# Kernel optimization log

Measured on AMD Instinct MI355X. Metric: run time of the kernel, lower is better.

Reference implementation:

```python
import jax, jax.numpy as jnp
import numpy as np

B, T = 16, 8192
L, RC, DC, SC, EC, E, NC = 16, 32, 32, 256, 256, 100, 256


def conv1d(x, w, b, dilation=1):
    # x: [B, Cin, T], w: [Cout, Cin, K], b: [Cout]
    y = jax.lax.conv_general_dilated(
        x, w, window_strides=(1,), padding='VALID',
        rhs_dilation=(dilation,), dimension_numbers=('NCH', 'OIH', 'NCH'))
    return y + b[None, :, None]


def setup_inputs() -> dict:
    key = jax.random.key(0)
    ks = jax.random.split(key, 32)
    n = lambda k, shp: (jax.random.normal(k, shp) * 0.1).astype(jnp.float32)
    return dict(
        tokens=jax.random.randint(ks[0], (B, T), 0, NC),
        emb=n(ks[1], (NC, E)),
        init_w=n(ks[2], (RC, E, 1)), init_b=n(ks[3], (RC,)),
        dil_w=n(ks[4], (L, DC, RC, 2)), dil_b=n(ks[5], (L, DC)),
        filt_w=n(ks[6], (L, DC, DC, 2)), filt_b=n(ks[7], (L, DC)),
        gate_w=n(ks[8], (L, DC, DC, 2)), gate_b=n(ks[9], (L, DC)),
        res_w=n(ks[10], (L, RC, DC, 1)), res_b=n(ks[11], (L, RC)),
        skip_w=n(ks[12], (L, SC, DC, 1)), skip_b=n(ks[13], (L, SC)),
        end1_w=n(ks[14], (EC, SC, 1)), end1_b=n(ks[15], (EC,)),
        end2_w=n(ks[16], (EC, EC, 1)), end2_b=n(ks[17], (EC,)),
        fc1_w=n(ks[18], (128, 256)), fc1_b=n(ks[19], (128,)),
        fc2_w=n(ks[20], (128, 128)), fc2_b=n(ks[21], (128,)),
        fc3_w=n(ks[22], (64, 128)), fc3_b=n(ks[23], (64,)),
        fc4_w=n(ks[24], (NC, 64)), fc4_b=n(ks[25], (NC,)),
    )


def reference(tokens, emb, init_w, init_b, dil_w, dil_b, filt_w, filt_b,
              gate_w, gate_b, res_w, res_b, skip_w, skip_b,
              end1_w, end1_b, end2_w, end2_b,
              fc1_w, fc1_b, fc2_w, fc2_b, fc3_w, fc3_b, fc4_w, fc4_b):
    x = emb[tokens]                     # [B, T, E]
    x = jnp.transpose(x, (0, 2, 1))     # [B, E, T]
    x = conv1d(x, init_w, init_b)       # [B, RC, T]
    skip = None
    for i in range(L):
        d = 2 ** (i % 4)                # dilation resets each block of 4 layers
        xp = jnp.pad(x, ((0, 0), (0, 0), (d + 1, 0)))        # left pad d+1
        residual = conv1d(xp, dil_w[i], dil_b[i], dilation=d)  # [B, DC, T+1]
        f = jnp.tanh(conv1d(residual, filt_w[i], filt_b[i]))   # [B, DC, T]
        g = jax.nn.sigmoid(conv1d(residual, gate_w[i], gate_b[i]))
        x = f * g
        skip = conv1d(x, skip_w[i], skip_b[i])   # overwritten each layer (source bug, kept faithful)
        x = conv1d(x, res_w[i], res_b[i]) + residual[:, :, :-1]
    h = jax.nn.relu(conv1d(jax.nn.relu(skip), end1_w, end1_b))
    h = conv1d(h, end2_w, end2_b)       # [B, EC, T]
    h = h[:, :, -1]                     # [B, 256] last timestep only
    h = jax.nn.relu(h @ fc1_w.T + fc1_b)
    h = jax.nn.relu(h @ fc2_w.T + fc2_b)
    h = jax.nn.relu(h @ fc3_w.T + fc3_b)
    out = h @ fc4_w.T + fc4_b           # [B, NC]
    return out
```

## Files before the change

kernel.cpp:

```cpp
#include <hip/hip_runtime.h>


#define BB 16
#define TT 8192
#define LL 16
#define W0 77
#define NT 256

typedef __attribute__((ext_vector_type(8)))  short short8;
typedef __attribute__((ext_vector_type(16))) float float16;

#define MFMA_B16(a, b, c) __builtin_amdgcn_mfma_f32_32x32x16_bf16(a, b, c, 0, 0, 0)

__device__ __forceinline__ short f2bs(float f) {
  union { float ff; unsigned u; } v; v.ff = f;
  unsigned u = v.u;
  return (short)((u + 0x7FFFu + ((u >> 16) & 1u)) >> 16);
}
__device__ __forceinline__ float b2f(short h) {
  union { unsigned u; float f; } v;
  v.u = ((unsigned)(unsigned short)h) << 16; return v.f;
}

__device__ __forceinline__ void afrag2(const short* src, int row, int kh, short8* out) {
  out[0] = *(const short8*)&src[row * 32 + 8 * kh];
  out[1] = *(const short8*)&src[row * 32 + 16 + 8 * kh];
}

__device__ __forceinline__ void load_chunk(
    int li, int cid, float* pf,
    const float* dil_w, const float* filt_w, const float* gate_w, const float* res_w)
{
  int mat = cid >> 7;
  int h = (cid >> 6) & 1, ln = cid & 63;
  int n = ln & 31, k2 = ln >> 5;
  int base = (li * 32 + n) * 32 + 16 * h + 8 * k2;
  if (mat == 6) {
    const float* p = res_w + base;
    #pragma unroll
    for (int j = 0; j < 8; j++) pf[j] = p[j];
  } else {
    const float* w = (mat < 2) ? dil_w : (mat < 4) ? filt_w : gate_w;
    const float* p = w + base * 2 + (mat & 1);
    #pragma unroll
    for (int j = 0; j < 8; j++) pf[j] = p[2 * j];
  }
}

__global__ __launch_bounds__(NT, 1) void wavenet_kernel(
    const int* __restrict__ tokens,
    const float* __restrict__ emb,
    const float* __restrict__ init_w, const float* __restrict__ init_b,
    const float* __restrict__ dil_w,  const float* __restrict__ dil_b,
    const float* __restrict__ filt_w, const float* __restrict__ filt_b,
    const float* __restrict__ gate_w, const float* __restrict__ gate_b,
    const float* __restrict__ res_w,  const float* __restrict__ res_b,
    const float* __restrict__ skip_w, const float* __restrict__ skip_b,
    const float* __restrict__ end1_w, const float* __restrict__ end1_b,
    const float* __restrict__ end2_w, const float* __restrict__ end2_b,
    const float* __restrict__ fc1_w,  const float* __restrict__ fc1_b,
    const float* __restrict__ fc2_w,  const float* __restrict__ fc2_b,
    const float* __restrict__ fc3_w,  const float* __restrict__ fc3_b,
    const float* __restrict__ fc4_w,  const float* __restrict__ fc4_b,
    float* __restrict__ out)
{
  __shared__ __align__(16) short bfw[2][7168];
  __shared__ float bias2[2][128];
  __shared__ __align__(16) short xbuf[W0 * 32];
  __shared__ __align__(16) short pool[8624];
  __shared__ int tok[W0];
  __shared__ __align__(16) float vecA[256], vecB[256];

  short* rb = pool;
  short* xm = pool + 2432;

  const int tid  = threadIdx.x;
  const int lane = tid & 63;
  const int wv   = tid >> 6;
  const int m    = lane & 31;
  const int kh   = lane >> 5;
  const int b    = blockIdx.x;

  if (tid < W0) tok[tid] = tokens[b * TT + (TT - 1 - tid)];
  __syncthreads();

  for (int cid = tid; cid < 77 * 14; cid += NT) {
    int u = cid / 14, s = cid % 14;
    const float* er = emb + tok[u] * 100 + s * 8;
    short8 v;
    if (s < 12) {
      #pragma unroll
      for (int j = 0; j < 8; j++) v[j] = f2bs(er[j]);
    } else if (s == 12) {
      #pragma unroll
      for (int j = 0; j < 4; j++) v[j] = f2bs(er[j]);
      #pragma unroll
      for (int j = 4; j < 8; j++) v[j] = 0;
    } else {
      #pragma unroll
      for (int j = 0; j < 8; j++) v[j] = 0;
    }
    *(short8*)&pool[u * 112 + s * 8] = v;
  }
  for (int cid = tid; cid < 896; cid += NT) {
    float pf[8];
    load_chunk(0, cid, pf, dil_w, filt_w, gate_w, res_w);
    short8 v;
    #pragma unroll
    for (int j = 0; j < 8; j++) v[j] = f2bs(pf[j]);
    *(short8*)&bfw[0][cid * 8] = v;
  }
  if (tid < 128) {
    const float* bsrc = (tid < 32) ? dil_b : (tid < 64) ? filt_b : (tid < 96) ? gate_b : res_b;
    bias2[0][tid] = bsrc[tid & 31];
  }
  __syncthreads();

  if (wv < 3) {
    short8 bi[7];
    #pragma unroll
    for (int s = 0; s < 7; s++) {
      const float* p = init_w + m * 100 + s * 16 + kh * 8;
      short8 v;
      if (s < 6) {
        #pragma unroll
        for (int j = 0; j < 8; j++) v[j] = f2bs(p[j]);
      } else if (kh == 0) {
        #pragma unroll
        for (int j = 0; j < 4; j++) v[j] = f2bs(p[j]);
        #pragma unroll
        for (int j = 4; j < 8; j++) v[j] = 0;
      } else {
        #pragma unroll
        for (int j = 0; j < 8; j++) v[j] = 0;
      }
      bi[s] = v;
    }
    const float binit = init_b[m];
    const int R = wv * 32;
    int u = R + m; if (u > 76) u = 76;
    float16 acc;
    #pragma unroll
    for (int r = 0; r < 16; r++) acc[r] = binit;
    #pragma unroll
    for (int s = 0; s < 7; s++) {
      short8 a = *(const short8*)&pool[u * 112 + s * 16 + kh * 8];
      acc = MFMA_B16(a, bi[s], acc);
    }
    #pragma unroll
    for (int r = 0; r < 16; r++) {
      int row = (r & 3) + 8 * (r >> 2) + 4 * kh;
      int uu = R + row;
      if (uu < W0) xbuf[uu * 32 + m] = f2bs(acc[r]);
    }
  }
  __syncthreads();

  int Win = W0;
  for (int i = 0; i < LL; i++) {
    const int d = 1 << (i & 3);
    const int Wout = Win - d - 1;
    const int T = (Wout + 32) >> 5;
    const short* bw = bfw[i & 1];
    const float* bs = bias2[i & 1];

    float pfo[4][8];
    float pbias = 0.f;
    const int nch = (tid < 128) ? 4 : 3;
    const bool oldpf = (T >= 3) && (i + 1 < LL);
    if (oldpf) {
      #pragma unroll
      for (int q = 0; q < 4; q++) {
        if (q < nch)
          load_chunk(i + 1, tid + q * NT, pfo[q], dil_w, filt_w, gate_w, res_w);
      }
      if (tid < 128) {
        const float* bsrc = (tid < 32) ? dil_b : (tid < 64) ? filt_b : (tid < 96) ? gate_b : res_b;
        pbias = bsrc[(i + 1) * 32 + (tid & 31)];
      }
    }
    const bool newpf = (T <= 2) && (i + 1 < LL) && (wv >= T);
    const int nP = NT - T * 64;
    const int ptid = tid - T * 64;
    float pfn[7][8];
    if (newpf) {
      #pragma unroll
      for (int q = 0; q < 7; q++) {
        int c = ptid + q * nP;
        if (c < 896) load_chunk(i + 1, c, pfn[q], dil_w, filt_w, gate_w, res_w);
      }
    }

    short8 BW[5][2];
    if (wv < T) {
      const int R = wv * 32;
      short8 B0[2], B1[2];
      #pragma unroll
      for (int h = 0; h < 2; h++) {
        B0[h] = *(const short8*)&bw[((0 * 2 + h) * 64 + lane) * 8];
        B1[h] = *(const short8*)&bw[((1 * 2 + h) * 64 + lane) * 8];
      }
      #pragma unroll
      for (int mt = 0; mt < 5; mt++)
        #pragma unroll
        for (int h = 0; h < 2; h++)
          BW[mt][h] = *(const short8*)&bw[(((mt + 2) * 2 + h) * 64 + lane) * 8];
      int vra = R + m + d; if (vra > Win - 1) vra = Win - 1;
      int vrz = R + m;     if (vrz > Win - 1) vrz = Win - 1;
      short8 aA[2], aZ[2];
      afrag2(xbuf, vra, kh, aA);
      afrag2(xbuf, vrz, kh, aZ);
      float16 acc;
      const float bc = bs[m];
      #pragma unroll
      for (int r = 0; r < 16; r++) acc[r] = bc;
      acc = MFMA_B16(aA[0], B0[0], acc);
      acc = MFMA_B16(aA[1], B0[1], acc);
      acc = MFMA_B16(aZ[0], B1[0], acc);
      acc = MFMA_B16(aZ[1], B1[1], acc);
      #pragma unroll
      for (int r = 0; r < 16; r++) {
        int row = (r & 3) + 8 * (r >> 2) + 4 * kh;
        int vr = R + row;
        if (vr <= Wout) rb[vr * 32 + m] = f2bs(acc[r]);
      }
    }
    if (T >= 2) {
      __syncthreads();
    } else {
      asm volatile("s_waitcnt lgkmcnt(0)" ::: "memory");
    }

    if (wv < T) {
      const int R = wv * 32;
      int r1 = R + m + 1; if (r1 > Wout) r1 = Wout;
      int r0 = R + m;     if (r0 > Wout) r0 = Wout;
      short8 a1[2], a0[2];
      afrag2(rb, r1, kh, a1);
      afrag2(rb, r0, kh, a0);
      float16 accF, accG;
      const float bf = bs[32 + m], bg = bs[64 + m];
      #pragma unroll
      for (int r = 0; r < 16; r++) { accF[r] = bf; accG[r] = bg; }
      accF = MFMA_B16(a1[0], BW[0][0], accF);
      accF = MFMA_B16(a1[1], BW[0][1], accF);
      accF = MFMA_B16(a0[0], BW[1][0], accF);
      accF = MFMA_B16(a0[1], BW[1][1], accF);
      accG = MFMA_B16(a1[0], BW[2][0], accG);
      accG = MFMA_B16(a1[1], BW[2][1], accG);
      accG = MFMA_B16(a0[0], BW[3][0], accG);
      accG = MFMA_B16(a0[1], BW[3][1], accG);
      #pragma unroll
      for (int r = 0; r < 16; r++) {
        int row = (r & 3) + 8 * (r >> 2) + 4 * kh;
        int uf = R + row;
        if (uf < Wout) {
          float u = __expf(-2.f * accF[r]);
          float v = __expf(-accG[r]);
          float fg = (1.f - u) * __builtin_amdgcn_rcpf((1.f + u) * (1.f + v));
          xm[uf * 32 + m] = f2bs(fg);
        }
      }
      asm volatile("s_waitcnt lgkmcnt(0)" ::: "memory");

      int rx = R + m; if (rx > Wout - 1) rx = Wout - 1;
      short8 aX[2];
      afrag2(xm, rx, kh, aX);
      float16 accX;
      const float br = bs[96 + m];
      #pragma unroll
      for (int r = 0; r < 16; r++) {
        int row = (r & 3) + 8 * (r >> 2) + 4 * kh;
        int rr = R + row + 1; if (rr > Wout) rr = Wout;
        accX[r] = br + b2f(rb[rr * 32 + m]);
      }
      accX = MFMA_B16(aX[0], BW[4][0], accX);
      accX = MFMA_B16(aX[1], BW[4][1], accX);
      #pragma unroll
      for (int r = 0; r < 16; r++) {
        int row = (r & 3) + 8 * (r >> 2) + 4 * kh;
        int uf = R + row;
        if (uf < Wout) xbuf[uf * 32 + m] = f2bs(accX[r]);
      }
    } else if (newpf) {
      short* dst = bfw[(i + 1) & 1];
      #pragma unroll
      for (int q = 0; q < 7; q++) {
        int c = ptid + q * nP;
        if (c < 896) {
          short8 v;
          #pragma unroll
          for (int j = 0; j < 8; j++) v[j] = f2bs(pfn[q][j]);
          *(short8*)&dst[c * 8] = v;
        }
      }
      for (int t2 = ptid; t2 < 128; t2 += nP) {
        const float* bsrc = (t2 < 32) ? dil_b : (t2 < 64) ? filt_b : (t2 < 96) ? gate_b : res_b;
        bias2[(i + 1) & 1][t2] = bsrc[(i + 1) * 32 + (t2 & 31)];
      }
    }

    if (oldpf) {
      short* dst = bfw[(i + 1) & 1];
      #pragma unroll
      for (int q = 0; q < 4; q++) {
        if (q < nch) {
          short8 v;
          #pragma unroll
          for (int j = 0; j < 8; j++) v[j] = f2bs(pfo[q][j]);
          *(short8*)&dst[(tid + q * NT) * 8] = v;
        }
      }
      if (tid < 128) bias2[(i + 1) & 1][tid] = pbias;
    }
    __syncthreads();
    Win = Wout;
  }

  {
    float acc = skip_b[15 * 256 + tid];
    const float* wr = skip_w + (15 * 256 + tid) * 32;
    #pragma unroll
    for (int k = 0; k < 32; k += 4) {
      float4 w = *(const float4*)&wr[k];
      acc += (w.x * b2f(xm[k]) + w.y * b2f(xm[k+1])) + (w.z * b2f(xm[k+2]) + w.w * b2f(xm[k+3]));
    }
    vecA[tid] = fmaxf(acc, 0.f);
  }
  __syncthreads();
  {
    const float* wr = end1_w + tid * 256;
    float a4[4] = {0.f, 0.f, 0.f, 0.f};
    #pragma unroll 4
    for (int k = 0; k < 256; k += 16) {
      #pragma unroll
      for (int q = 0; q < 4; q++) {
        float4 w = *(const float4*)&wr[k + 4 * q];
        float4 a = *(const float4*)&vecA[k + 4 * q];
        a4[q] += (w.x * a.x + w.y * a.y) + (w.z * a.z + w.w * a.w);
      }
    }
    vecB[tid] = fmaxf(end1_b[tid] + (a4[0] + a4[1]) + (a4[2] + a4[3]), 0.f);
  }
  __syncthreads();
  float h2;
  {
    const float* wr = end2_w + tid * 256;
    float a4[4] = {0.f, 0.f, 0.f, 0.f};
    #pragma unroll 4
    for (int k = 0; k < 256; k += 16) {
      #pragma unroll
      for (int q = 0; q < 4; q++) {
        float4 w = *(const float4*)&wr[k + 4 * q];
        float4 a = *(const float4*)&vecB[k + 4 * q];
        a4[q] += (w.x * a.x + w.y * a.y) + (w.z * a.z + w.w * a.w);
      }
    }
    h2 = end2_b[tid] + (a4[0] + a4[1]) + (a4[2] + a4[3]);
  }
  __syncthreads();
  vecA[tid] = h2;
  __syncthreads();
  if (tid < 128) {
    const float* wr = fc1_w + tid * 256;
    float a4[4] = {0.f, 0.f, 0.f, 0.f};
    #pragma unroll 4
    for (int k = 0; k < 256; k += 16) {
      #pragma unroll
      for (int q = 0; q < 4; q++) {
        float4 w = *(const float4*)&wr[k + 4 * q];
        float4 a = *(const float4*)&vecA[k + 4 * q];
        a4[q] += (w.x * a.x + w.y * a.y) + (w.z * a.z + w.w * a.w);
      }
    }
    vecB[tid] = fmaxf(fc1_b[tid] + (a4[0] + a4[1]) + (a4[2] + a4[3]), 0.f);
  }
  __syncthreads();
  if (tid < 128) {
    const float* wr = fc2_w + tid * 128;
    float a4[4] = {0.f, 0.f, 0.f, 0.f};
    #pragma unroll 2
    for (int k = 0; k < 128; k += 16) {
      #pragma unroll
      for (int q = 0; q < 4; q++) {
        float4 w = *(const float4*)&wr[k + 4 * q];
        float4 a = *(const float4*)&vecB[k + 4 * q];
        a4[q] += (w.x * a.x + w.y * a.y) + (w.z * a.z + w.w * a.w);
      }
    }
    vecA[tid] = fmaxf(fc2_b[tid] + (a4[0] + a4[1]) + (a4[2] + a4[3]), 0.f);
  }
  __syncthreads();
  if (tid < 64) {
    const float* wr = fc3_w + tid * 128;
    float a4[4] = {0.f, 0.f, 0.f, 0.f};
    #pragma unroll 2
    for (int k = 0; k < 128; k += 16) {
      #pragma unroll
      for (int q = 0; q < 4; q++) {
        float4 w = *(const float4*)&wr[k + 4 * q];
        float4 a = *(const float4*)&vecA[k + 4 * q];
        a4[q] += (w.x * a.x + w.y * a.y) + (w.z * a.z + w.w * a.w);
      }
    }
    vecB[tid] = fmaxf(fc3_b[tid] + (a4[0] + a4[1]) + (a4[2] + a4[3]), 0.f);
  }
  __syncthreads();
  {
    const float* wr = fc4_w + tid * 64;
    float a4[4] = {0.f, 0.f, 0.f, 0.f};
    #pragma unroll
    for (int k = 0; k < 64; k += 16) {
      #pragma unroll
      for (int q = 0; q < 4; q++) {
        float4 w = *(const float4*)&wr[k + 4 * q];
        float4 a = *(const float4*)&vecB[k + 4 * q];
        a4[q] += (w.x * a.x + w.y * a.y) + (w.z * a.z + w.w * a.w);
      }
    }
    out[b * 256 + tid] = fc4_b[tid] + (a4[0] + a4[1]) + (a4[2] + a4[3]);
  }
}

extern "C" void kernel_launch(void* const* d_in, const int* in_sizes, int n_in,
                              void* d_out, int out_size, void* d_ws, size_t ws_size,
                              hipStream_t stream) {
  wavenet_kernel<<<BB, NT, 0, stream>>>(
      (const int*)d_in[0],    (const float*)d_in[1],  (const float*)d_in[2],  (const float*)d_in[3],
      (const float*)d_in[4],  (const float*)d_in[5],  (const float*)d_in[6],  (const float*)d_in[7],
      (const float*)d_in[8],  (const float*)d_in[9],  (const float*)d_in[10], (const float*)d_in[11],
      (const float*)d_in[12], (const float*)d_in[13], (const float*)d_in[14], (const float*)d_in[15],
      (const float*)d_in[16], (const float*)d_in[17], (const float*)d_in[18], (const float*)d_in[19],
      (const float*)d_in[20], (const float*)d_in[21], (const float*)d_in[22], (const float*)d_in[23],
      (const float*)d_in[24], (const float*)d_in[25], (float*)d_out);
}
```

Measured before the change: 208.4 us.

## Run last five WaveNet layers in one wavefront with register shuffles

The final five layers now run in a specialized path. When the window is 32 timesteps or fewer, wave 0 holds activations in registers and passes time-shifted operands between lanes with shuffles and packed bf16 conversions, so no LDS round trips are needed. The other three waves prefetch and convert the next layer's weights and biases in parallel. This aims to cut LDS traffic and barrier latency on the small tail layers. The risk is heavy register pressure and leaving the other waves idle during the compute.

```diff
diff --git a/kernel.cpp b/kernel.cpp
--- a/kernel.cpp
+++ b/kernel.cpp
@@ -20,6 +20,28 @@
 __device__ __forceinline__ float b2f(short h) {
   union { unsigned u; float f; } v;
   v.u = ((unsigned)(unsigned short)h) << 16; return v.f;
+}
+__device__ __forceinline__ unsigned cvtpk(float lo, float hi) {
+  unsigned r;
+  asm("v_cvt_pk_bf16_f32 %0, %1, %2" : "=v"(r) : "v"(lo), "v"(hi));
+  return r;
+}
+__device__ __forceinline__ short8 mk8(unsigned a, unsigned b, unsigned c, unsigned d) {
+  union { unsigned u[4]; short8 s; } z;
+  z.u[0] = a; z.u[1] = b; z.u[2] = c; z.u[3] = d; return z.s;
+}
+__device__ __forceinline__ float u2f(unsigned u) {
+  union { unsigned x; float f; } z; z.x = u; return z.f;
+}
+__device__ __forceinline__ void asmb(const unsigned* own, const unsigned* cr,
+                                     int kh, unsigned* o) {
+  #pragma unroll
+  for (int h = 0; h < 2; h++) {
+    o[4*h+0] = kh ? cr[4*h+2] : own[4*h+0];
+    o[4*h+1] = kh ? cr[4*h+3] : own[4*h+1];
+    o[4*h+2] = kh ? own[4*h+2] : cr[4*h+0];
+    o[4*h+3] = kh ? own[4*h+3] : cr[4*h+1];
+  }
 }
 
 __device__ __forceinline__ void afrag2(const short* src, int row, int kh, short8* out) {
@@ -65,7 +87,7 @@
     float* __restrict__ out)
 {
   __shared__ __align__(16) short bfw[2][7168];
-  __shared__ float bias2[2][128];
+  __shared__ __align__(16) float bias2[2][128];
   __shared__ __align__(16) short xbuf[W0 * 32];
   __shared__ __align__(16) short pool[8624];
   __shared__ int tok[W0];
@@ -157,7 +179,7 @@
   __syncthreads();
 
   int Win = W0;
-  for (int i = 0; i < LL; i++) {
+  for (int i = 0; i < 11; i++) {
     const int d = 1 << (i & 3);
     const int Wout = Win - d - 1;
     const int T = (Wout + 32) >> 5;
@@ -315,6 +337,167 @@
     }
     __syncthreads();
     Win = Wout;
+  }
+
+  {
+    const int t31 = lane & 31;
+    const int hb  = lane & 32;
+    unsigned xcur[8];
+    if (wv == 0) {
+      int tcl = t31 < Win - 1 ? t31 : Win - 1;
+      #pragma unroll
+      for (int h = 0; h < 2; h++) {
+        short8 v = *(const short8*)&xbuf[tcl * 32 + 16 * h + 8 * kh];
+        union { short8 s; unsigned u[4]; } z; z.s = v;
+        #pragma unroll
+        for (int s = 0; s < 4; s++) xcur[4 * h + s] = z.u[s];
+      }
+    }
+
+    #pragma unroll
+    for (int i = 11; i < LL; i++) {
+      const int d = 1 << (i & 3);
+      const int Wout = Win - d - 1;
+      const short* bw = bfw[i & 1];
+      const float* bs = bias2[i & 1];
+
+      const bool npf = (i + 1 < LL) && (wv >= 1);
+      const int ptid = tid - 64;
+      float pfn[7][8];
+      if (npf) {
+        #pragma unroll
+        for (int q = 0; q < 7; q++) {
+          int c = ptid + q * 192;
+          if (c < 896) load_chunk(i + 1, c, pfn[q], dil_w, filt_w, gate_w, res_w);
+        }
+      }
+
+      if (wv == 0) {
+        short8 WA[7][2];
+        #pragma unroll
+        for (int mt = 0; mt < 7; mt++)
+          #pragma unroll
+          for (int h = 0; h < 2; h++)
+            WA[mt][h] = *(const short8*)&bw[((mt * 2 + h) * 64 + lane) * 8];
+
+        int td = t31 + d; if (td > Win - 1) td = Win - 1;
+        int srcd = hb | td;
+        unsigned xd[8];
+        #pragma unroll
+        for (int q = 0; q < 8; q++) xd[q] = (unsigned)__shfl((int)xcur[q], srcd);
+        float16 acc;
+        #pragma unroll
+        for (int g = 0; g < 4; g++) {
+          float4 b4 = *(const float4*)&bs[4 * kh + 8 * g];
+          acc[4*g+0] = b4.x; acc[4*g+1] = b4.y; acc[4*g+2] = b4.z; acc[4*g+3] = b4.w;
+        }
+        acc = MFMA_B16(WA[0][0], mk8(xd[0], xd[1], xd[2], xd[3]), acc);
+        acc = MFMA_B16(WA[0][1], mk8(xd[4], xd[5], xd[6], xd[7]), acc);
+        acc = MFMA_B16(WA[1][0], mk8(xcur[0], xcur[1], xcur[2], xcur[3]), acc);
+        acc = MFMA_B16(WA[1][1], mk8(xcur[4], xcur[5], xcur[6], xcur[7]), acc);
+
+        unsigned wrb[8], xc[8], x1[8], x1c[8];
+        #pragma unroll
+        for (int q = 0; q < 8; q++) wrb[q] = cvtpk(acc[2 * q], acc[2 * q + 1]);
+        int t1 = t31 + 1; if (t1 > Wout) t1 = Wout;
+        int s1o = hb | t1;
+        int s1c = (hb ^ 32) | t1;
+        #pragma unroll
+        for (int q = 0; q < 8; q++) {
+          xc[q]  = (unsigned)__shfl((int)wrb[q], lane ^ 32);
+          x1[q]  = (unsigned)__shfl((int)wrb[q], s1o);
+          x1c[q] = (unsigned)__shfl((int)wrb[q], s1c);
+        }
+        unsigned rb0w[8], rb1w[8];
+        asmb(wrb, xc, kh, rb0w);
+        asmb(x1, x1c, kh, rb1w);
+
+        float16 accF, accG;
+        #pragma unroll
+        for (int g = 0; g < 4; g++) {
+          float4 bF = *(const float4*)&bs[32 + 4 * kh + 8 * g];
+          float4 bG = *(const float4*)&bs[64 + 4 * kh + 8 * g];
+          accF[4*g+0] = bF.x; accF[4*g+1] = bF.y; accF[4*g+2] = bF.z; accF[4*g+3] = bF.w;
+          accG[4*g+0] = bG.x; accG[4*g+1] = bG.y; accG[4*g+2] = bG.z; accG[4*g+3] = bG.w;
+        }
+        short8 RB10 = mk8(rb1w[0], rb1w[1], rb1w[2], rb1w[3]);
+        short8 RB11 = mk8(rb1w[4], rb1w[5], rb1w[6], rb1w[7]);
+        short8 RB00 = mk8(rb0w[0], rb0w[1], rb0w[2], rb0w[3]);
+        short8 RB01 = mk8(rb0w[4], rb0w[5], rb0w[6], rb0w[7]);
+        accF = MFMA_B16(WA[2][0], RB10, accF);
+        accF = MFMA_B16(WA[2][1], RB11, accF);
+        accF = MFMA_B16(WA[3][0], RB00, accF);
+        accF = MFMA_B16(WA[3][1], RB01, accF);
+        accG = MFMA_B16(WA[4][0], RB10, accG);
+        accG = MFMA_B16(WA[4][1], RB11, accG);
+        accG = MFMA_B16(WA[5][0], RB00, accG);
+        accG = MFMA_B16(WA[5][1], RB01, accG);
+        float fg[16];
+        #pragma unroll
+        for (int r = 0; r < 16; r++) {
+          float u = __expf(-2.f * accF[r]);
+          float v = __expf(-accG[r]);
+          fg[r] = (1.f - u) * __builtin_amdgcn_rcpf((1.f + u) * (1.f + v));
+        }
+        unsigned wxm[8];
+        #pragma unroll
+        for (int q = 0; q < 8; q++) wxm[q] = cvtpk(fg[2 * q], fg[2 * q + 1]);
+
+        if (i == LL - 1) {
+          if (t31 == 0) {
+            #pragma unroll
+            for (int q = 0; q < 8; q++) {
+              int c0 = (2 * q & 3) + 8 * (q >> 1) + 4 * kh;
+              *(unsigned*)&xm[c0] = wxm[q];
+            }
+          }
+        } else {
+          unsigned xmc[8];
+          #pragma unroll
+          for (int q = 0; q < 8; q++) xmc[q] = (unsigned)__shfl((int)wxm[q], lane ^ 32);
+          unsigned xmw[8];
+          asmb(wxm, xmc, kh, xmw);
+          float16 accX;
+          #pragma unroll
+          for (int g = 0; g < 4; g++) {
+            float4 bR = *(const float4*)&bs[96 + 4 * kh + 8 * g];
+            #pragma unroll
+            for (int j = 0; j < 4; j++) {
+              int r = 4 * g + j;
+              unsigned w = x1[r >> 1];
+              float rv = (r & 1) ? u2f(w & 0xFFFF0000u) : u2f(w << 16);
+              accX[r] = ((const float*)&bR)[j] + rv;
+            }
+          }
+          accX = MFMA_B16(WA[6][0], mk8(xmw[0], xmw[1], xmw[2], xmw[3]), accX);
+          accX = MFMA_B16(WA[6][1], mk8(xmw[4], xmw[5], xmw[6], xmw[7]), accX);
+          unsigned wxn[8], xnc[8];
+          #pragma unroll
+          for (int q = 0; q < 8; q++) wxn[q] = cvtpk(accX[2 * q], accX[2 * q + 1]);
+          #pragma unroll
+          for (int q = 0; q < 8; q++) xnc[q] = (unsigned)__shfl((int)wxn[q], lane ^ 32);
+          asmb(wxn, xnc, kh, xcur);
+        }
+      } else if (npf) {
+        short* dst = bfw[(i + 1) & 1];
+        #pragma unroll
+        for (int q = 0; q < 7; q++) {
+          int c = ptid + q * 192;
+          if (c < 896) {
+            short8 v;
+            #pragma unroll
+            for (int j = 0; j < 8; j++) v[j] = f2bs(pfn[q][j]);
+            *(short8*)&dst[c * 8] = v;
+          }
+        }
+        for (int t2 = ptid; t2 < 128; t2 += 192) {
+          const float* bsrc = (t2 < 32) ? dil_b : (t2 < 64) ? filt_b : (t2 < 96) ? gate_b : res_b;
+          bias2[(i + 1) & 1][t2] = bsrc[(i + 1) * 32 + (t2 & 31)];
+        }
+      }
+      __syncthreads();
+      Win = Wout;
+    }
   }
 
   {
```

Measured after the change: 205.0 us. About the same (-1.7%).
